# Performance work log

Hardware: AMD Instinct MI355X
Metric: run time of the kernel (lower is better)

## Reference

```python
import jax, jax.numpy as jnp
import numpy as np

N, T, D, H = 100000, 16, 8, 40
HP1 = H + 1
ALPHA_DP = 1.0
KAPPA0 = 1000.0   # priorGaussianVarKappa
NU0 = 100.0       # priorWishartNu
PSI0_SCALE = 500.0  # priorWishartPsi = 500*I


def setup_inputs() -> dict:
    key = jax.random.key(0)
    ks = jax.random.split(key, 6)
    return {
        "BetaGamma1": jnp.ones((1, T), jnp.float32),
        "Phi": jax.random.uniform(ks[0], (N, T), jnp.float32),
        "inputData": jax.random.normal(ks[1], (N, D), jnp.float32),
        "outputData": jax.random.normal(ks[2], (N, 1), jnp.float32),
        "weightELM": jax.random.uniform(ks[3], (D, H), jnp.float32) * 2.0 - 1.0,
        "biasELM": jax.random.normal(ks[4], (H, 1), jnp.float32),
        "epsilonA": jnp.ones((1, T), jnp.float32),
        "epsilonB": jnp.ones((1, T), jnp.float32),
        "zetaA": 1e-4 * jnp.ones((1, T), jnp.float32),
        "zetaB": jnp.ones((1, T), jnp.float32),
    }


def reference(BetaGamma1, Phi, inputData, outputData, weightELM, biasELM,
              epsilonA, epsilonB, zetaA, zetaB):
    f32 = jnp.float32
    mu0 = jnp.zeros((D, 1), f32)                      # priorGaussianMeanMu
    Psi0 = PSI0_SCALE * jnp.eye(D, dtype=f32)         # priorWishartPsi

    sumPhi = jnp.sum(Phi, axis=0, keepdims=True)      # [1,T]

    # stick-breaking Beta params. Torch builds a flipped [T,N,T] tril mask;
    # mathematically BetaGamma2[t] = alpha + sum_{j>t} sum_n Phi[n,j]
    BetaGamma1_new = jnp.ones_like(BetaGamma1) + sumPhi
    col = sumPhi[0]                                   # [T]
    rev_incl = jnp.cumsum(col[::-1])[::-1]            # sum_{j>=t}
    BetaGamma2 = (ALPHA_DP + (rev_incl - col))[None, :]

    # Gaussian-Wishart natural-parameter updates.
    # Torch loops over clusters doing [N,D,D] bmm outer products; this is
    # S[:,:,t] = sum_n Phi[n,t] x_n x_n^T
    S = jnp.einsum('nt,ni,nj->ijt', Phi, inputData, inputData)  # [D,D,T]
    t11 = -0.5 * (Psi0 + KAPPA0 * mu0 @ mu0.T)[:, :, None] - 0.5 * S
    t12 = KAPPA0 * mu0 + inputData.T @ Phi            # [D,T]
    t21 = -0.5 * sumPhi - 0.5 * (NU0 + D + 2)         # [1,T]
    kappa = KAPPA0 + sumPhi                           # [1,T]
    mu = t12 / kappa                                  # [D,T]
    nu = -2.0 * t21 - 2.0 - float(D)                  # [1,T]
    psi = -2.0 * t11 - kappa[0][None, None, :] * jnp.einsum('it,jt->ijt', mu, mu)

    # ELM feature map + augmented design matrix X = [sigmoid(x W + b), 1]
    hmap = jax.nn.sigmoid(inputData @ weightELM + biasELM.T)   # [N,H]
    X = jnp.concatenate([hmap, jnp.ones((inputData.shape[0], 1), f32)], axis=1)  # [N,HP1]

    epsExp = (epsilonA / epsilonB)[0]                 # [T]
    zetaExp = (zetaA / zetaB)[0]                      # [T]

    # A[t] = X^T diag(Phi[:,t]) X   (torch: per-cluster bmm with diag_embed)
    A = jnp.einsum('nt,ni,nj->tij', Phi, X, X)        # [T,HP1,HP1]
    WS = jnp.linalg.inv(epsExp[:, None, None] * A
                        + zetaExp[:, None, None] * jnp.eye(HP1, dtype=f32))
    # b[t] = X^T diag(Phi[:,t]) y
    b = jnp.einsum('ni,nt->ti', X * outputData, Phi)  # [T,HP1]
    WMv = zetaExp[:, None] * jnp.einsum('tij,tj->ti', WS, b)   # [T,HP1]
    WM = WMv[:, :, None]                              # [T,HP1,1]

    # prior Zeta/Epsilon alias the variational initial values in __init__
    zetaA_new = zetaA + (H + 1) * 0.5
    zetaB_new = zetaB + 0.5 * (jnp.sum(WMv * WMv, axis=1)
                               + jnp.trace(WS, axis1=-2, axis2=-1))[None, :]
    epsA_new = epsilonA + 0.5 * sumPhi

    pred = jnp.einsum('ni,ti->tn', X, WMv)            # [T,N]
    err = outputData.T - pred                          # [T,N]
    t1 = jnp.einsum('tn,nt->t', err * err, Phi)[None, :]
    t2 = jnp.einsum('tij,tji->t', A, WS)[None, :]
    epsB_new = epsilonB + 0.5 * (t1 + t2)

    return (BetaGamma1_new, BetaGamma2, mu, kappa, nu, psi,
            WM, WS, zetaA_new, zetaB_new, epsA_new, epsB_new)
```

## Files before the change

kernel.cpp:

```cpp
#include <hip/hip_runtime.h>

#define Nn 100000
#define Tt 16
#define Dd 8
#define Hh 40
#define HP1 41

#define CSZ 53248
#define KCMAX 125
#define XE_PAIR_OFF 0
#define XE_PAIR_SZ  (Nn * 64)
#define PART_OFF    (XE_PAIR_OFF + XE_PAIR_SZ)
#define PART_SZ     (16 * CSZ)
#define P_OFF       (PART_OFF + PART_SZ)

#define OFF_BG1   0
#define OFF_BG2   16
#define OFF_MU    32
#define OFF_KAPPA 160
#define OFF_NU    176
#define OFF_PSI   192
#define OFF_WM    1216
#define OFF_WS    1872
#define OFF_ZA    28768
#define OFF_ZB    28784
#define OFF_EA    28800
#define OFF_EB    28816

typedef _Float16 f16x8 __attribute__((ext_vector_type(8)));
typedef float f32x4 __attribute__((ext_vector_type(4)));
typedef unsigned short u16x8 __attribute__((ext_vector_type(8)));

#define AIDX(i, t, j) ((((i) * 16 + (t)) * 64) + (j))

__global__ __launch_bounds__(256)
void elm_expand(const float* __restrict__ Xd, const float* __restrict__ Yd,
                const float* __restrict__ W, const float* __restrict__ bb,
                unsigned int* __restrict__ XePair)
{
  __shared__ float sW[Dd * Hh];
  __shared__ float sb[Hh];
  __shared__ float xs[64][9];
  __shared__ float ys[64];
  __shared__ float hrow[64][41];
  int tid = threadIdx.x;
  int n0 = blockIdx.x * 64;

  for (int i = tid; i < Dd * Hh; i += 256) sW[i] = W[i];
  if (tid < Hh) sb[tid] = bb[tid];
  if (tid < 128) {
    int nl = tid >> 1, h4 = (tid & 1) * 4;
    int gn = n0 + nl;
    float4 v = (gn < Nn) ? *(const float4*)(Xd + (size_t)gn * 8 + h4)
                         : make_float4(0.f, 0.f, 0.f, 0.f);
    xs[nl][h4 + 0] = v.x; xs[nl][h4 + 1] = v.y;
    xs[nl][h4 + 2] = v.z; xs[nl][h4 + 3] = v.w;
  }
  if (tid < 64) { int gn = n0 + tid; ys[tid] = (gn < Nn) ? Yd[gn] : 0.f; }
  __syncthreads();

  {
    int nl = tid >> 2, hq = (tid & 3) * 10;
    for (int hh = 0; hh < 10; ++hh) {
      int h = hq + hh;
      float z = sb[h];
#pragma unroll
      for (int d = 0; d < 8; ++d) z = fmaf(xs[nl][d], sW[d * Hh + h], z);
      hrow[nl][h] = 1.f / (1.f + __expf(-z));
    }
  }
  __syncthreads();

  for (int pass = 0; pass < 16; ++pass) {
    int idx = pass * 256 + tid;
    int nl = idx >> 6, cc = idx & 63;
    int gn = n0 + nl;
    if (gn < Nn) {
      float v = (cc < Hh) ? hrow[nl][cc]
              : (cc == 40) ? 1.f
              : (cc < 49) ? xs[nl][cc - 41]
              : (cc == 49) ? ys[nl] : 0.f;
      _Float16 hi = (_Float16)v;
      _Float16 lo = (_Float16)(v - (float)hi);
      unsigned int u = ((unsigned int)__builtin_bit_cast(unsigned short, lo) << 16)
                     |  (unsigned int)__builtin_bit_cast(unsigned short, hi);
      XePair[(size_t)gn * 64 + cc] = u;
    }
  }
}

__device__ __forceinline__ float pair_to_f32(unsigned int u) {
  _Float16 hi = __builtin_bit_cast(_Float16, (unsigned short)(u & 0xffffu));
  _Float16 lo = __builtin_bit_cast(_Float16, (unsigned short)(u >> 16));
  return (float)hi + (float)lo;
}

__global__ __launch_bounds__(256, 2)
void gram_mfma(const float* __restrict__ Phi, const unsigned int* __restrict__ XePair,
               float* __restrict__ P, int CH)
{
  int tid = threadIdx.x;
  int lane = tid & 63;
  int wave = tid >> 6;
  int wg_n = wave & 1;
  int wg_m = wave >> 1;
  int l15 = lane & 15, lg = lane >> 4;
  int bM = blockIdx.x;
  int c  = blockIdx.y;
  int n0 = c * CH;
  int nEnd = n0 + CH; if (nEnd > Nn) nEnd = Nn;
  int i0 = bM * 13 + wg_m * 7;
  int jB = wg_n * 32 + l15;

  f32x4 acc[7][2];
#pragma unroll
  for (int m = 0; m < 7; ++m) {
    acc[m][0] = (f32x4){0.f, 0.f, 0.f, 0.f};
    acc[m][1] = (f32x4){0.f, 0.f, 0.f, 0.f};
  }

  for (int nb = n0; nb < nEnd; nb += 32) {
    int kb = nb + lg * 8;

    float ph[8];
#pragma unroll
    for (int e = 0; e < 8; ++e) ph[e] = Phi[(size_t)(kb + e) * 16 + l15];

    f16x8 bh[2], bl[2];
#pragma unroll
    for (int nt = 0; nt < 2; ++nt) {
      u16x8 vh, vl;
#pragma unroll
      for (int e = 0; e < 8; ++e) {
        unsigned int u = XePair[(size_t)(kb + e) * 64 + jB + nt * 16];
        vh[e] = (unsigned short)(u & 0xffffu);
        vl[e] = (unsigned short)(u >> 16);
      }
      bh[nt] = __builtin_bit_cast(f16x8, vh);
      bl[nt] = __builtin_bit_cast(f16x8, vl);
    }

#pragma unroll
    for (int mt = 0; mt < 7; ++mt) {
      int iA = i0 + mt;
      f16x8 ah, al;
#pragma unroll
      for (int e = 0; e < 8; ++e) {
        unsigned int u = XePair[(size_t)(kb + e) * 64 + iA];
        float a = ph[e] * pair_to_f32(u);
        _Float16 h = (_Float16)a;
        ah[e] = h;
        al[e] = (_Float16)(a - (float)h);
      }
#pragma unroll
      for (int nt = 0; nt < 2; ++nt) {
        acc[mt][nt] = __builtin_amdgcn_mfma_f32_16x16x32_f16(ah, bh[nt], acc[mt][nt], 0, 0, 0);
        acc[mt][nt] = __builtin_amdgcn_mfma_f32_16x16x32_f16(ah, bl[nt], acc[mt][nt], 0, 0, 0);
        acc[mt][nt] = __builtin_amdgcn_mfma_f32_16x16x32_f16(al, bh[nt], acc[mt][nt], 0, 0, 0);
      }
    }
  }

  int ntile = (wg_m == 1) ? 6 : 7;
  float* Pc = P + (size_t)c * CSZ;
#pragma unroll
  for (int mt = 0; mt < 7; ++mt) {
    if (mt >= ntile) break;
    int iA = i0 + mt;
#pragma unroll
    for (int nt = 0; nt < 2; ++nt) {
      int j = wg_n * 32 + nt * 16 + l15;
#pragma unroll
      for (int r = 0; r < 4; ++r) {
        Pc[(iA * 16 + (lg * 4 + r)) * 64 + j] = acc[mt][nt][r];
      }
    }
  }
}

__global__ __launch_bounds__(256)
void reduce_chunks(const float4* __restrict__ P4, int nchunks, float4* __restrict__ part4)
{
  int g = blockIdx.y;
  int idx = blockIdx.x * 256 + threadIdx.x;
  int per = (nchunks + 15) / 16;
  int c0 = g * per;
  int c1 = c0 + per; if (c1 > nchunks) c1 = nchunks;
  float4 s = make_float4(0.f, 0.f, 0.f, 0.f);
  for (int cc = c0; cc < c1; ++cc) {
    float4 v = P4[(size_t)cc * (CSZ / 4) + idx];
    s.x += v.x; s.y += v.y; s.z += v.z; s.w += v.w;
  }
  part4[(size_t)g * (CSZ / 4) + idx] = s;
}

__device__ __forceinline__ float accv(const float* __restrict__ part, int idx) {
  float s = 0.f;
#pragma unroll
  for (int g = 0; g < 16; ++g) s += part[g * CSZ + idx];
  return s;
}

__global__ __launch_bounds__(256)
void finalize_kernel(const float* __restrict__ part, const float* __restrict__ epsA,
                     const float* __restrict__ epsB, const float* __restrict__ zetA,
                     const float* __restrict__ zetB, float* __restrict__ out)
{
  int t = blockIdx.x;
  int tid = threadIdx.x;
  __shared__ float G[HP1][84];
  __shared__ float As[HP1][HP1 + 1];
  __shared__ float bs[HP1];
  __shared__ float colk[HP1];
  __shared__ float red[256];
  __shared__ float wmv[HP1];
  __shared__ float rowv[4][HP1 + 1];
  __shared__ float mus[Dd];

  float epsExp = epsA[t] / epsB[t];
  float zetaExp = zetA[t] / zetB[t];

  for (int idx = tid; idx < HP1 * HP1; idx += 256) {
    int i = idx / HP1, j = idx % HP1;
    float a = accv(part, AIDX(i, t, j));
    As[i][j] = a;
    G[i][j] = epsExp * a + (i == j ? zetaExp : 0.f);
    G[i][41 + j] = (i == j) ? 1.f : 0.f;
  }
  for (int idx = tid; idx < HP1; idx += 256) {
    G[idx][82] = 0.f; G[idx][83] = 0.f;
    bs[idx] = accv(part, AIDX(idx, t, 49));
  }
  __syncthreads();

  int c = tid % HP1;
  int ig = tid / HP1;
  int irow0 = ig * 7;

  for (int k = 0; k < HP1; ++k) {
    float pivinv = 1.f / G[k][k];
    if (tid >= 1 && tid <= HP1) G[k][k + tid] *= pivinv;
    if (tid < HP1) colk[tid] = (tid == k) ? 0.f : G[tid][k];
    __syncthreads();
    if (ig < 6) {
      int j = k + 1 + c;
      float pk = G[k][j];
#pragma unroll
      for (int r = 0; r < 7; ++r) {
        int i = irow0 + r;
        if (i < HP1 && i != k) G[i][j] = fmaf(-colk[i], pk, G[i][j]);
      }
    }
    __syncthreads();
  }

  for (int idx = tid; idx < HP1 * HP1; idx += 256) {
    int i = idx / HP1, j = idx % HP1;
    out[OFF_WS + (t * HP1 + i) * HP1 + j] = G[i][41 + j];
  }
  if (tid < HP1) {
    float s = 0.f;
    for (int j = 0; j < HP1; ++j) s += G[tid][41 + j] * bs[j];
    float w = zetaExp * s;
    wmv[tid] = w;
    out[OFF_WM + t * HP1 + tid] = w;
  }
  __syncthreads();
  float lt2 = 0.f;
  for (int idx = tid; idx < HP1 * HP1; idx += 256) {
    int i = idx / HP1, j = idx % HP1;
    lt2 += As[i][j] * G[i][41 + j];
  }
  red[tid] = lt2; __syncthreads();
  for (int s = 128; s > 0; s >>= 1) {
    if (tid < s) red[tid] += red[tid + s];
    __syncthreads();
  }
  float t2v = red[0];
  if (tid < HP1) {
    float w = wmv[tid];
    float aw = 0.f;
    for (int j = 0; j < HP1; ++j) aw += As[tid][j] * wmv[j];
    rowv[0][tid] = w * bs[tid];
    rowv[1][tid] = w * w;
    rowv[2][tid] = G[tid][41 + tid];
    rowv[3][tid] = w * aw;
  }
  __syncthreads();

  float sp = accv(part, AIDX(40, t, 40));
  float kap = 1000.f + sp;
  float syy = accv(part, AIDX(49, t, 49));

  if (tid == 0) {
    float wb = 0.f, wn = 0.f, trc = 0.f, quad = 0.f;
    for (int i = 0; i < HP1; ++i) {
      wb += rowv[0][i]; wn += rowv[1][i]; trc += rowv[2][i]; quad += rowv[3][i];
    }
    float t1 = syy - 2.f * wb + quad;
    out[OFF_BG1 + t] = 1.f + sp;
    float rest = 0.f;
    for (int u = t + 1; u < Tt; ++u) rest += accv(part, AIDX(40, u, 40));
    out[OFF_BG2 + t] = 1.f + rest;
    out[OFF_KAPPA + t] = kap;
    out[OFF_NU + t] = sp + 100.f;
    out[OFF_ZA + t] = zetA[t] + 0.5f * (float)HP1;
    out[OFF_ZB + t] = zetB[t] + 0.5f * (wn + trc);
    out[OFF_EA + t] = epsA[t] + 0.5f * sp;
    out[OFF_EB + t] = epsB[t] + 0.5f * (t1 + t2v);
  }
  if (tid < Dd) {
    float m = accv(part, AIDX(40, t, 41 + tid)) / kap;
    mus[tid] = m;
    out[OFF_MU + tid * Tt + t] = m;
  }
  __syncthreads();
  if (tid < Dd * Dd) {
    int i = tid / Dd, j = tid % Dd;
    float S = accv(part, AIDX(41 + i, t, 41 + j));
    float v = (i == j ? 500.f : 0.f) + S - kap * mus[i] * mus[j];
    out[OFF_PSI + (i * Dd + j) * Tt + t] = v;
  }
}

extern "C" void kernel_launch(void* const* d_in, const int* in_sizes, int n_in,
                              void* d_out, int out_size, void* d_ws, size_t ws_size,
                              hipStream_t stream) {
  const float* Phi = (const float*)d_in[1];
  const float* Xd  = (const float*)d_in[2];
  const float* Yd  = (const float*)d_in[3];
  const float* W   = (const float*)d_in[4];
  const float* bb  = (const float*)d_in[5];
  const float* eA  = (const float*)d_in[6];
  const float* eB  = (const float*)d_in[7];
  const float* zA  = (const float*)d_in[8];
  const float* zB  = (const float*)d_in[9];
  float* out = (float*)d_out;
  float* ws  = (float*)d_ws;

  unsigned int* XePair = (unsigned int*)(ws + XE_PAIR_OFF);
  float* part = ws + PART_OFF;
  float* P    = ws + P_OFF;

  long maxChunks = ((long)(ws_size / 4) - (long)P_OFF) / CSZ;
  int mch = 1;
  while (mch < KCMAX && (long)((KCMAX + mch - 1) / mch) > maxChunks) ++mch;
  int CH = 800 * mch;
  int KCe = (Nn + CH - 1) / CH;

  hipLaunchKernelGGL(elm_expand, dim3((Nn + 63) / 64), dim3(256), 0, stream,
                     Xd, Yd, W, bb, XePair);
  hipLaunchKernelGGL(gram_mfma, dim3(4, KCe), dim3(256), 0, stream,
                     Phi, XePair, P, CH);
  hipLaunchKernelGGL(reduce_chunks, dim3(52, 16), dim3(256), 0, stream,
                     (const float4*)P, KCe, (float4*)part);
  hipLaunchKernelGGL(finalize_kernel, dim3(Tt), dim3(256), 0, stream,
                     part, eA, eB, zA, zB, out);
}
```

Baseline: 202.3 us.

## Transpose Xe and Phi to column-major and stage gram tiles through LDS

The expand kernel now writes the hi/lo-split features and Phi in feature-major (transposed) layout. The gram kernel uses double-buffered global_load_lds staging with XOR-swizzled LDS reads, and each wave covers 4 row tiles by 4 column tiles instead of direct strided global loads. The chunk reduction is split into two stages, so finalize reads one summed buffer instead of 16 partials. The intent is coalesced loads and fewer redundant global reads. The cost is an extra Phi transpose, an extra kernel launch, and a chunk size that varies with workspace size.

```diff
diff --git a/kernel.cpp b/kernel.cpp
--- a/kernel.cpp
+++ b/kernel.cpp
@@ -7,12 +7,13 @@
 #define HP1 41
 
 #define CSZ 53248
-#define KCMAX 125
-#define XE_PAIR_OFF 0
-#define XE_PAIR_SZ  (Nn * 64)
-#define PART_OFF    (XE_PAIR_OFF + XE_PAIR_SZ)
-#define PART_SZ     (16 * CSZ)
-#define P_OFF       (PART_OFF + PART_SZ)
+#define XET_OFF  0
+#define XET_SZ   (64 * Nn)
+#define PHIT_OFF (XET_OFF + XET_SZ)
+#define PHIT_SZ  (16 * Nn)
+#define ACC_OFF  (PHIT_OFF + PHIT_SZ)
+#define PART_OFF (ACC_OFF + CSZ)
+#define P_OFF    (PART_OFF + 8 * CSZ)
 
 #define OFF_BG1   0
 #define OFF_BG2   16
@@ -30,19 +31,22 @@
 typedef _Float16 f16x8 __attribute__((ext_vector_type(8)));
 typedef float f32x4 __attribute__((ext_vector_type(4)));
 typedef unsigned short u16x8 __attribute__((ext_vector_type(8)));
+typedef unsigned int u32x4 __attribute__((ext_vector_type(4)));
 
 #define AIDX(i, t, j) ((((i) * 16 + (t)) * 64) + (j))
 
 __global__ __launch_bounds__(256)
-void elm_expand(const float* __restrict__ Xd, const float* __restrict__ Yd,
-                const float* __restrict__ W, const float* __restrict__ bb,
-                unsigned int* __restrict__ XePair)
+void elm_expand(const float* __restrict__ Phi, const float* __restrict__ Xd,
+                const float* __restrict__ Yd, const float* __restrict__ W,
+                const float* __restrict__ bb, unsigned int* __restrict__ XeT,
+                float* __restrict__ PhiT)
 {
   __shared__ float sW[Dd * Hh];
   __shared__ float sb[Hh];
   __shared__ float xs[64][9];
   __shared__ float ys[64];
   __shared__ float hrow[64][41];
+  __shared__ float pt[16][68];
   int tid = threadIdx.x;
   int n0 = blockIdx.x * 64;
 
@@ -57,8 +61,15 @@
     xs[nl][h4 + 2] = v.z; xs[nl][h4 + 3] = v.w;
   }
   if (tid < 64) { int gn = n0 + tid; ys[tid] = (gn < Nn) ? Yd[gn] : 0.f; }
-  __syncthreads();
-
+  {
+    int nl = tid >> 2, q = tid & 3;
+    int gn = n0 + nl;
+    float4 v = (gn < Nn) ? *(const float4*)(Phi + (size_t)gn * 16 + q * 4)
+                         : make_float4(0.f, 0.f, 0.f, 0.f);
+    pt[q * 4 + 0][nl] = v.x; pt[q * 4 + 1][nl] = v.y;
+    pt[q * 4 + 2][nl] = v.z; pt[q * 4 + 3][nl] = v.w;
+  }
+  __syncthreads();
   {
     int nl = tid >> 2, hq = (tid & 3) * 10;
     for (int hh = 0; hh < 10; ++hh) {
@@ -70,122 +81,191 @@
     }
   }
   __syncthreads();
-
-  for (int pass = 0; pass < 16; ++pass) {
-    int idx = pass * 256 + tid;
-    int nl = idx >> 6, cc = idx & 63;
-    int gn = n0 + nl;
+  {
+    int t = tid & 15, nq = tid >> 4;
+    int gn = n0 + nq * 4;
     if (gn < Nn) {
-      float v = (cc < Hh) ? hrow[nl][cc]
-              : (cc == 40) ? 1.f
-              : (cc < 49) ? xs[nl][cc - 41]
-              : (cc == 49) ? ys[nl] : 0.f;
-      _Float16 hi = (_Float16)v;
-      _Float16 lo = (_Float16)(v - (float)hi);
-      unsigned int u = ((unsigned int)__builtin_bit_cast(unsigned short, lo) << 16)
-                     |  (unsigned int)__builtin_bit_cast(unsigned short, hi);
-      XePair[(size_t)gn * 64 + cc] = u;
-    }
-  }
-}
-
-__device__ __forceinline__ float pair_to_f32(unsigned int u) {
-  _Float16 hi = __builtin_bit_cast(_Float16, (unsigned short)(u & 0xffffu));
-  _Float16 lo = __builtin_bit_cast(_Float16, (unsigned short)(u >> 16));
-  return (float)hi + (float)lo;
+      float4 v = make_float4(pt[t][nq * 4 + 0], pt[t][nq * 4 + 1],
+                             pt[t][nq * 4 + 2], pt[t][nq * 4 + 3]);
+      *(float4*)(PhiT + (size_t)t * Nn + gn) = v;
+    }
+  }
+  {
+    int c = tid >> 2, nb = (tid & 3) * 16;
+    for (int q = 0; q < 4; ++q) {
+      int nl = nb + q * 4;
+      int gn = n0 + nl;
+      if (gn >= Nn) break;
+      unsigned int pu[4];
+#pragma unroll
+      for (int j = 0; j < 4; ++j) {
+        int n = nl + j;
+        float v;
+        if (c < Hh) v = hrow[n][c];
+        else if (c == 40) v = 1.f;
+        else if (c < 49) v = xs[n][c - 41];
+        else if (c == 49) v = ys[n];
+        else v = 0.f;
+        _Float16 hi = (_Float16)v;
+        _Float16 lo = (_Float16)(v - (float)hi);
+        pu[j] = ((unsigned int)__builtin_bit_cast(unsigned short, lo) << 16)
+              |  (unsigned int)__builtin_bit_cast(unsigned short, hi);
+      }
+      *(uint4*)(XeT + (size_t)c * Nn + gn) =
+          make_uint4(pu[0], pu[1], pu[2], pu[3]);
+    }
+  }
+}
+
+__device__ __forceinline__ void gload16(const void* g, void* l) {
+  __builtin_amdgcn_global_load_lds(
+      (const __attribute__((address_space(1))) unsigned int*)g,
+      (__attribute__((address_space(3))) unsigned int*)l, 16, 0, 0);
+}
+
+__device__ __forceinline__ void unpack8(u32x4 a, u32x4 b, f16x8& hi, f16x8& lo) {
+  u16x8 vh, vl;
+#pragma unroll
+  for (int e = 0; e < 4; ++e) {
+    vh[e] = (unsigned short)(a[e] & 0xffffu);
+    vl[e] = (unsigned short)(a[e] >> 16);
+    vh[4 + e] = (unsigned short)(b[e] & 0xffffu);
+    vl[4 + e] = (unsigned short)(b[e] >> 16);
+  }
+  hi = __builtin_bit_cast(f16x8, vh);
+  lo = __builtin_bit_cast(f16x8, vl);
+}
+
+__device__ __forceinline__ void buildA(u32x4 a, u32x4 b, const float* ph,
+                                       f16x8& ah, f16x8& al) {
+  unsigned int u8[8];
+#pragma unroll
+  for (int e = 0; e < 4; ++e) { u8[e] = a[e]; u8[4 + e] = b[e]; }
+#pragma unroll
+  for (int e = 0; e < 8; ++e) {
+    unsigned int u = u8[e];
+    float hi = (float)__builtin_bit_cast(_Float16, (unsigned short)(u & 0xffffu));
+    float lo = (float)__builtin_bit_cast(_Float16, (unsigned short)(u >> 16));
+    float v = ph[e] * (hi + lo);
+    _Float16 h = (_Float16)v;
+    ah[e] = h;
+    al[e] = (_Float16)(v - (float)h);
+  }
 }
 
 __global__ __launch_bounds__(256, 2)
-void gram_mfma(const float* __restrict__ Phi, const unsigned int* __restrict__ XePair,
+void gram_mfma(const float* __restrict__ PhiT, const unsigned int* __restrict__ XeT,
                float* __restrict__ P, int CH)
 {
+  __shared__ __align__(16) unsigned int xe_lds[2][2048];
+  __shared__ __align__(16) float phi_lds[2][512];
+
   int tid = threadIdx.x;
-  int lane = tid & 63;
-  int wave = tid >> 6;
-  int wg_n = wave & 1;
-  int wg_m = wave >> 1;
-  int l15 = lane & 15, lg = lane >> 4;
-  int bM = blockIdx.x;
-  int c  = blockIdx.y;
+  int l = tid & 63, w = tid >> 6;
+  int lr = l >> 3, lp = l & 7;
+  int gsw = lp ^ lr;
+  int l15 = l & 15, lg = l >> 4;
+  int bM = blockIdx.x, c = blockIdx.y;
   int n0 = c * CH;
-  int nEnd = n0 + CH; if (nEnd > Nn) nEnd = Nn;
-  int i0 = bM * 13 + wg_m * 7;
-  int jB = wg_n * 32 + l15;
-
-  f32x4 acc[7][2];
-#pragma unroll
-  for (int m = 0; m < 7; ++m) {
-    acc[m][0] = (f32x4){0.f, 0.f, 0.f, 0.f};
-    acc[m][1] = (f32x4){0.f, 0.f, 0.f, 0.f};
-  }
-
-  for (int nb = n0; nb < nEnd; nb += 32) {
-    int kb = nb + lg * 8;
-
-    float ph[8];
-#pragma unroll
-    for (int e = 0; e < 8; ++e) ph[e] = Phi[(size_t)(kb + e) * 16 + l15];
-
-    f16x8 bh[2], bl[2];
-#pragma unroll
-    for (int nt = 0; nt < 2; ++nt) {
-      u16x8 vh, vl;
-#pragma unroll
-      for (int e = 0; e < 8; ++e) {
-        unsigned int u = XePair[(size_t)(kb + e) * 64 + jB + nt * 16];
-        vh[e] = (unsigned short)(u & 0xffffu);
-        vl[e] = (unsigned short)(u >> 16);
+  int rem = Nn - n0; if (rem > CH) rem = CH;
+  int nsteps = rem >> 5;
+  int i0 = bM * 13;
+
+  const unsigned int* gx0 = XeT + (size_t)(16 * w + lr) * Nn + n0 + 4 * gsw;
+  const unsigned int* gx1 = XeT + (size_t)(16 * w + 8 + lr) * Nn + n0 + 4 * gsw;
+  const float* gp = PhiT + (size_t)(8 * w + lr) * Nn + n0 + 4 * gsw;
+
+#define STAGE(nxt) do {                                   \
+    gload16(gx0, &xe_lds[nxt][(2 * w) * 256]);            \
+    gload16(gx1, &xe_lds[nxt][(2 * w + 1) * 256]);        \
+    if (w < 2) gload16(gp, &phi_lds[nxt][w * 256]);       \
+    gx0 += 32; gx1 += 32; gp += 32;                       \
+  } while (0)
+
+  int s1 = (2 * lg) ^ (l15 & 7), s2 = (2 * lg + 1) ^ (l15 & 7);
+  int off_p0 = (l15 * 32 + 4 * s1) * 4, off_p1 = (l15 * 32 + 4 * s2) * 4;
+  int off_b0[4], off_b1[4];
+#pragma unroll
+  for (int nt = 0; nt < 4; ++nt) {
+    off_b0[nt] = ((l15 + 16 * nt) * 32 + 4 * s1) * 4;
+    off_b1[nt] = ((l15 + 16 * nt) * 32 + 4 * s2) * 4;
+  }
+  int off_a0[4], off_a1[4];
+#pragma unroll
+  for (int mi = 0; mi < 4; ++mi) {
+    int i = i0 + 4 * w + mi;
+    int a1 = (2 * lg) ^ (i & 7), a2 = (2 * lg + 1) ^ (i & 7);
+    off_a0[mi] = (i * 32 + 4 * a1) * 4;
+    off_a1[mi] = (i * 32 + 4 * a2) * 4;
+  }
+
+  f32x4 acc[4][4];
+#pragma unroll
+  for (int mi = 0; mi < 4; ++mi)
+#pragma unroll
+    for (int nt = 0; nt < 4; ++nt) acc[mi][nt] = (f32x4){0.f, 0.f, 0.f, 0.f};
+
+  STAGE(0);
+  __syncthreads();
+
+  for (int s = 0; s < nsteps; ++s) {
+    int cur = s & 1;
+    if (s + 1 < nsteps) STAGE(cur ^ 1);
+
+    const char* xb = (const char*)&xe_lds[cur][0];
+    const char* pb = (const char*)&phi_lds[cur][0];
+    f32x4 p0 = *(const f32x4*)(pb + off_p0);
+    f32x4 p1 = *(const f32x4*)(pb + off_p1);
+    float ph[8] = {p0[0], p0[1], p0[2], p0[3], p1[0], p1[1], p1[2], p1[3]};
+
+    f16x8 bh[4], bl[4];
+#pragma unroll
+    for (int nt = 0; nt < 4; ++nt) {
+      u32x4 lo4 = *(const u32x4*)(xb + off_b0[nt]);
+      u32x4 hi4 = *(const u32x4*)(xb + off_b1[nt]);
+      unpack8(lo4, hi4, bh[nt], bl[nt]);
+    }
+#pragma unroll
+    for (int mi = 0; mi < 4; ++mi) {
+      u32x4 a0 = *(const u32x4*)(xb + off_a0[mi]);
+      u32x4 a1 = *(const u32x4*)(xb + off_a1[mi]);
+      f16x8 ah, al;
+      buildA(a0, a1, ph, ah, al);
+#pragma unroll
+      for (int nt = 0; nt < 4; ++nt) {
+        acc[mi][nt] = __builtin_amdgcn_mfma_f32_16x16x32_f16(ah, bh[nt], acc[mi][nt], 0, 0, 0);
+        acc[mi][nt] = __builtin_amdgcn_mfma_f32_16x16x32_f16(ah, bl[nt], acc[mi][nt], 0, 0, 0);
+        acc[mi][nt] = __builtin_amdgcn_mfma_f32_16x16x32_f16(al, bh[nt], acc[mi][nt], 0, 0, 0);
       }
-      bh[nt] = __builtin_bit_cast(f16x8, vh);
-      bl[nt] = __builtin_bit_cast(f16x8, vl);
-    }
-
-#pragma unroll
-    for (int mt = 0; mt < 7; ++mt) {
-      int iA = i0 + mt;
-      f16x8 ah, al;
-#pragma unroll
-      for (int e = 0; e < 8; ++e) {
-        unsigned int u = XePair[(size_t)(kb + e) * 64 + iA];
-        float a = ph[e] * pair_to_f32(u);
-        _Float16 h = (_Float16)a;
-        ah[e] = h;
-        al[e] = (_Float16)(a - (float)h);
+    }
+    __syncthreads();
+  }
+#undef STAGE
+
+  float* Pc = P + (size_t)c * CSZ;
+#pragma unroll
+  for (int mi = 0; mi < 4; ++mi) {
+    int mloc = 4 * w + mi;
+    if (mloc < 13) {
+      int i = i0 + mloc;
+#pragma unroll
+      for (int nt = 0; nt < 4; ++nt) {
+        int j = nt * 16 + l15;
+#pragma unroll
+        for (int r = 0; r < 4; ++r)
+          Pc[(i * 16 + lg * 4 + r) * 64 + j] = acc[mi][nt][r];
       }
-#pragma unroll
-      for (int nt = 0; nt < 2; ++nt) {
-        acc[mt][nt] = __builtin_amdgcn_mfma_f32_16x16x32_f16(ah, bh[nt], acc[mt][nt], 0, 0, 0);
-        acc[mt][nt] = __builtin_amdgcn_mfma_f32_16x16x32_f16(ah, bl[nt], acc[mt][nt], 0, 0, 0);
-        acc[mt][nt] = __builtin_amdgcn_mfma_f32_16x16x32_f16(al, bh[nt], acc[mt][nt], 0, 0, 0);
-      }
-    }
-  }
-
-  int ntile = (wg_m == 1) ? 6 : 7;
-  float* Pc = P + (size_t)c * CSZ;
-#pragma unroll
-  for (int mt = 0; mt < 7; ++mt) {
-    if (mt >= ntile) break;
-    int iA = i0 + mt;
-#pragma unroll
-    for (int nt = 0; nt < 2; ++nt) {
-      int j = wg_n * 32 + nt * 16 + l15;
-#pragma unroll
-      for (int r = 0; r < 4; ++r) {
-        Pc[(iA * 16 + (lg * 4 + r)) * 64 + j] = acc[mt][nt][r];
-      }
     }
   }
 }
 
 __global__ __launch_bounds__(256)
-void reduce_chunks(const float4* __restrict__ P4, int nchunks, float4* __restrict__ part4)
+void reduce_a(const float4* __restrict__ P4, int nchunks, float4* __restrict__ part4)
 {
   int g = blockIdx.y;
   int idx = blockIdx.x * 256 + threadIdx.x;
-  int per = (nchunks + 15) / 16;
-  int c0 = g * per;
-  int c1 = c0 + per; if (c1 > nchunks) c1 = nchunks;
+  int per = (nchunks + 7) / 8;
+  int c0 = g * per, c1 = c0 + per; if (c1 > nchunks) c1 = nchunks;
   float4 s = make_float4(0.f, 0.f, 0.f, 0.f);
   for (int cc = c0; cc < c1; ++cc) {
     float4 v = P4[(size_t)cc * (CSZ / 4) + idx];
@@ -194,15 +274,21 @@
   part4[(size_t)g * (CSZ / 4) + idx] = s;
 }
 
-__device__ __forceinline__ float accv(const float* __restrict__ part, int idx) {
-  float s = 0.f;
-#pragma unroll
-  for (int g = 0; g < 16; ++g) s += part[g * CSZ + idx];
-  return s;
-}
-
 __global__ __launch_bounds__(256)
-void finalize_kernel(const float* __restrict__ part, const float* __restrict__ epsA,
+void reduce_b(const float4* __restrict__ part4, float4* __restrict__ acc4)
+{
+  int idx = blockIdx.x * 256 + threadIdx.x;
+  float4 s = make_float4(0.f, 0.f, 0.f, 0.f);
+#pragma unroll
+  for (int g = 0; g < 8; ++g) {
+    float4 v = part4[(size_t)g * (CSZ / 4) + idx];
+    s.x += v.x; s.y += v.y; s.z += v.z; s.w += v.w;
+  }
+  acc4[idx] = s;
+}
+
+__global__ __launch_bounds__(256)
+void finalize_kernel(const float* __restrict__ acc, const float* __restrict__ epsA,
                      const float* __restrict__ epsB, const float* __restrict__ zetA,
                      const float* __restrict__ zetB, float* __restrict__ out)
 {
@@ -222,14 +308,14 @@
 
   for (int idx = tid; idx < HP1 * HP1; idx += 256) {
     int i = idx / HP1, j = idx % HP1;
-    float a = accv(part, AIDX(i, t, j));
+    float a = acc[AIDX(i, t, j)];
     As[i][j] = a;
     G[i][j] = epsExp * a + (i == j ? zetaExp : 0.f);
     G[i][41 + j] = (i == j) ? 1.f : 0.f;
   }
   for (int idx = tid; idx < HP1; idx += 256) {
     G[idx][82] = 0.f; G[idx][83] = 0.f;
-    bs[idx] = accv(part, AIDX(idx, t, 49));
+    bs[idx] = acc[AIDX(idx, t, 49)];
   }
   __syncthreads();
 
@@ -288,9 +374,9 @@
   }
   __syncthreads();
 
-  float sp = accv(part, AIDX(40, t, 40));
+  float sp = acc[AIDX(40, t, 40)];
   float kap = 1000.f + sp;
-  float syy = accv(part, AIDX(49, t, 49));
+  float syy = acc[AIDX(49, t, 49)];
 
   if (tid == 0) {
     float wb = 0.f, wn = 0.f, trc = 0.f, quad = 0.f;
@@ -300,7 +386,7 @@
     float t1 = syy - 2.f * wb + quad;
     out[OFF_BG1 + t] = 1.f + sp;
     float rest = 0.f;
-    for (int u = t + 1; u < Tt; ++u) rest += accv(part, AIDX(40, u, 40));
+    for (int u = t + 1; u < Tt; ++u) rest += acc[AIDX(40, u, 40)];
     out[OFF_BG2 + t] = 1.f + rest;
     out[OFF_KAPPA + t] = kap;
     out[OFF_NU + t] = sp + 100.f;
@@ -310,14 +396,14 @@
     out[OFF_EB + t] = epsB[t] + 0.5f * (t1 + t2v);
   }
   if (tid < Dd) {
-    float m = accv(part, AIDX(40, t, 41 + tid)) / kap;
+    float m = acc[AIDX(40, t, 41 + tid)] / kap;
     mus[tid] = m;
     out[OFF_MU + tid * Tt + t] = m;
   }
   __syncthreads();
   if (tid < Dd * Dd) {
     int i = tid / Dd, j = tid % Dd;
-    float S = accv(part, AIDX(41 + i, t, 41 + j));
+    float S = acc[AIDX(41 + i, t, 41 + j)];
     float v = (i == j ? 500.f : 0.f) + S - kap * mus[i] * mus[j];
     out[OFF_PSI + (i * Dd + j) * Tt + t] = v;
   }
@@ -338,22 +424,27 @@
   float* out = (float*)d_out;
   float* ws  = (float*)d_ws;
 
-  unsigned int* XePair = (unsigned int*)(ws + XE_PAIR_OFF);
-  float* part = ws + PART_OFF;
-  float* P    = ws + P_OFF;
+  unsigned int* XeT = (unsigned int*)(ws + XET_OFF);
+  float* PhiT    = ws + PHIT_OFF;
+  float* acc_red = ws + ACC_OFF;
+  float* part    = ws + PART_OFF;
+  float* P       = ws + P_OFF;
 
   long maxChunks = ((long)(ws_size / 4) - (long)P_OFF) / CSZ;
-  int mch = 1;
-  while (mch < KCMAX && (long)((KCMAX + mch - 1) / mch) > maxChunks) ++mch;
-  int CH = 800 * mch;
+  if (maxChunks < 1) maxChunks = 1;
+  long sp = (3125 + maxChunks - 1) / maxChunks;
+  if (sp < 13) sp = 13;
+  int CH = (int)(32 * sp);
   int KCe = (Nn + CH - 1) / CH;
 
   hipLaunchKernelGGL(elm_expand, dim3((Nn + 63) / 64), dim3(256), 0, stream,
-                     Xd, Yd, W, bb, XePair);
+                     Phi, Xd, Yd, W, bb, XeT, PhiT);
   hipLaunchKernelGGL(gram_mfma, dim3(4, KCe), dim3(256), 0, stream,
-                     Phi, XePair, P, CH);
-  hipLaunchKernelGGL(reduce_chunks, dim3(52, 16), dim3(256), 0, stream,
+                     PhiT, XeT, P, CH);
+  hipLaunchKernelGGL(reduce_a, dim3(52, 8), dim3(256), 0, stream,
                      (const float4*)P, KCe, (float4*)part);
+  hipLaunchKernelGGL(reduce_b, dim3(52), dim3(256), 0, stream,
+                     (const float4*)part, (float4*)acc_red);
   hipLaunchKernelGGL(finalize_kernel, dim3(Tt), dim3(256), 0, stream,
-                     part, eA, eB, zA, zB, out);
-}
+                     acc_red, eA, eB, zA, zB, out);
+}
```

Result: faster. 186.0 us (-8.1%).
